# Kernel tuning notes

Hardware: AMD Instinct MI355X
Metric: run time of the kernel (lower is better)

## Reference

```python
import jax, jax.numpy as jnp
import numpy as np

N, E, IN, HID, HEADS, OUT = 20000, 320000, 128, 64, 8, 64
NEG_SLOPE = 0.2  # PyG GATConv default leaky_relu slope


def setup_inputs() -> dict:
    key = jax.random.key(0)
    ks = jax.random.split(key, 12)
    g = lambda k, shape, fan_in: jax.random.normal(k, shape, jnp.float32) / np.sqrt(fan_in)
    return {
        "x": jax.random.normal(ks[0], (N, IN), jnp.float32),
        "edge_index": jax.random.randint(ks[1], (2, E), 0, N, jnp.int32),
        "W1": g(ks[2], (IN, HEADS * HID), IN),
        "att_src1": g(ks[3], (HEADS, HID), HID),
        "att_dst1": g(ks[4], (HEADS, HID), HID),
        "b1": jnp.zeros((HEADS * HID,), jnp.float32),
        "W2": g(ks[5], (HEADS * HID, OUT), HEADS * HID),
        "att_src2": g(ks[6], (1, OUT), OUT),
        "att_dst2": g(ks[7], (1, OUT), OUT),
        "b2": jnp.zeros((OUT,), jnp.float32),
    }


def gat_conv(x, edge_index, W, att_src, att_dst, b, heads, out_ch):
    """PyG-style GATConv with add_self_loops=True, concat=True."""
    n = x.shape[0]
    loop = jnp.arange(n, dtype=edge_index.dtype)
    src = jnp.concatenate([edge_index[0], loop])  # message source nodes
    dst = jnp.concatenate([edge_index[1], loop])  # aggregation targets

    h = (x @ W).reshape(n, heads, out_ch)               # [N,H,C]
    a_s = jnp.sum(h * att_src[None], axis=-1)            # [N,H]
    a_d = jnp.sum(h * att_dst[None], axis=-1)            # [N,H]

    e = jax.nn.leaky_relu(a_s[src] + a_d[dst], NEG_SLOPE)  # [Etot,H]
    # numerically stable edge-softmax over incoming neighborhoods
    m = jax.ops.segment_max(e, dst, num_segments=n)
    m = jnp.where(jnp.isfinite(m), m, 0.0)
    p = jnp.exp(e - m[dst])
    denom = jax.ops.segment_sum(p, dst, num_segments=n)
    alpha = p / denom[dst]                               # [Etot,H]

    out = jax.ops.segment_sum(h[src] * alpha[:, :, None], dst, num_segments=n)  # [N,H,C]
    return out.reshape(n, heads * out_ch) + b


def reference(x, edge_index, W1, att_src1, att_dst1, b1, W2, att_src2, att_dst2, b2):
    h = gat_conv(x, edge_index, W1, att_src1, att_dst1, b1, HEADS, HID)
    h = jax.nn.relu(h)
    out = gat_conv(h, edge_index, W2, att_src2, att_dst2, b2, 1, OUT)
    return out
```

## Files before the change

### kernel.cpp

```cpp
#include <hip/hip_runtime.h>
#include <cstdint>

#define N_NODES 20000
#define N_EDGES 320000
#define ET (N_EDGES + N_NODES)
#define IN_DIM 128
#define HID 64
#define HEADS 8
#define F1 (HEADS * HID)
#define OUT_DIM 64
#define NEG_SLOPE 0.2f
#define NB_SCAN 20

typedef __attribute__((ext_vector_type(8))) short bf16x8;
typedef __attribute__((ext_vector_type(4))) float f32x4;

__device__ __forceinline__ ushort f2bf(float f) {
  uint32_t u = __float_as_uint(f);
  uint32_t r = (u + 0x7fffu + ((u >> 16) & 1u)) >> 16;
  return (ushort)r;
}
__device__ __forceinline__ float bfu_lo(uint32_t p) { return __uint_as_float(p << 16); }
__device__ __forceinline__ float bfu_hi(uint32_t p) { return __uint_as_float(p & 0xffff0000u); }
__device__ __forceinline__ float lrelu(float x) { return x > 0.f ? x : NEG_SLOPE * x; }

__global__ void castT_kernel(const float* __restrict__ in, ushort* __restrict__ out,
                             int R, int C) {
  int idx = blockIdx.x * 256 + threadIdx.x;
  if (idx >= R * C) return;
  int r = idx / C, c = idx - r * C;
  out[(size_t)c * R + r] = f2bf(in[idx]);
}

__global__ void hist_kernel(const int* __restrict__ ei, int* __restrict__ deg) {
  int e = blockIdx.x * 256 + threadIdx.x;
  if (e >= ET) return;
  int dst = (e < N_EDGES) ? ei[N_EDGES + e] : (e - N_EDGES);
  atomicAdd(&deg[dst], 1);
}

__global__ __launch_bounds__(1024) void scan_a(const int* __restrict__ deg,
                                               int* __restrict__ off,
                                               int* __restrict__ bsum) {
  __shared__ int wsum[16];
  int i = blockIdx.x * 1024 + threadIdx.x;
  int lane = threadIdx.x & 63, wid = threadIdx.x >> 6;
  int v = (i < N_NODES) ? deg[i] : 0;
  int s = v;
#pragma unroll
  for (int d = 1; d < 64; d <<= 1) {
    int u = __shfl_up(s, d);
    if (lane >= d) s += u;
  }
  if (lane == 63) wsum[wid] = s;
  __syncthreads();
  if (wid == 0) {
    int ws = (lane < 16) ? wsum[lane] : 0;
#pragma unroll
    for (int d = 1; d < 16; d <<= 1) {
      int u = __shfl_up(ws, d);
      if (lane >= d) ws += u;
    }
    if (lane < 16) wsum[lane] = ws;
  }
  __syncthreads();
  int wbase = (wid > 0) ? wsum[wid - 1] : 0;
  int incl = wbase + s;
  if (i < N_NODES) off[i] = incl - v;
  if (threadIdx.x == 1023) bsum[blockIdx.x] = incl;
}

__global__ void scan_b(const int* __restrict__ bsum, int* __restrict__ boff,
                       int* __restrict__ off) {
  int lane = threadIdx.x;
  int orig = (lane < NB_SCAN) ? bsum[lane] : 0;
  int v = orig;
#pragma unroll
  for (int d = 1; d < 64; d <<= 1) {
    int u = __shfl_up(v, d);
    if (lane >= d) v += u;
  }
  if (lane < NB_SCAN) boff[lane] = v - orig;
  if (lane == NB_SCAN - 1) off[N_NODES] = v;
}

__global__ __launch_bounds__(1024) void scan_c(const int* __restrict__ boff,
                                               int* __restrict__ off,
                                               int* __restrict__ pos) {
  int i = blockIdx.x * 1024 + threadIdx.x;
  if (i >= N_NODES) return;
  int o = off[i] + boff[blockIdx.x];
  off[i] = o;
  pos[i] = o;
}

__global__ void scatter_kernel(const int* __restrict__ ei, int* __restrict__ pos,
                               int* __restrict__ csr_src) {
  int e = blockIdx.x * 256 + threadIdx.x;
  if (e >= ET) return;
  int src, dst;
  if (e < N_EDGES) { src = ei[e]; dst = ei[N_EDGES + e]; }
  else             { src = e - N_EDGES; dst = src; }
  int slot = atomicAdd(&pos[dst], 1);
  csr_src[slot] = src;
}

__device__ __forceinline__ int swz(int r, int kg) { return kg ^ ((r >> 1) & 3); }

template <int WR, int WC, int TM, int TN, int ASD, bool AF32>
__global__ __launch_bounds__(256) void gemm_kernel(
    const void* __restrict__ Av, const ushort* __restrict__ BT,
    ushort* __restrict__ Cb, int M, int K, int NC,
    const float* __restrict__ atts, const float* __restrict__ attd,
    float* __restrict__ asd) {
  constexpr int BM = WR * TM * 16;
  constexpr int BN = WC * TN * 16;
  __shared__ ushort As[BM * 32];
  __shared__ ushort Bs[BN * 32];
  const int t = threadIdx.x;
  const int lane = t & 63, wid = t >> 6;
  const int wr = wid / WC, wc = wid % WC;
  const int m0 = blockIdx.y * BM, n0 = blockIdx.x * BN;
  f32x4 acc[TM][TN] = {};
  const int srow = t >> 2, kg = t & 3;

  for (int k0 = 0; k0 < K; k0 += 32) {
#pragma unroll
    for (int q = 0; q < BM / 64; ++q) {
      int r = srow + 64 * q;
      int gr = m0 + r; if (gr >= M) gr = M - 1;
      bf16x8 v;
      if constexpr (AF32) {
        const float* Ap = (const float*)Av;
        float4 v0 = *reinterpret_cast<const float4*>(&Ap[(size_t)gr * K + k0 + kg * 8]);
        float4 v1 = *reinterpret_cast<const float4*>(&Ap[(size_t)gr * K + k0 + kg * 8 + 4]);
        v[0] = (short)f2bf(v0.x); v[1] = (short)f2bf(v0.y);
        v[2] = (short)f2bf(v0.z); v[3] = (short)f2bf(v0.w);
        v[4] = (short)f2bf(v1.x); v[5] = (short)f2bf(v1.y);
        v[6] = (short)f2bf(v1.z); v[7] = (short)f2bf(v1.w);
      } else {
        v = *reinterpret_cast<const bf16x8*>(&((const ushort*)Av)[(size_t)gr * K + k0 + kg * 8]);
      }
      *reinterpret_cast<bf16x8*>(&As[r * 32 + swz(r, kg) * 8]) = v;
    }
#pragma unroll
    for (int q = 0; q < BN / 64; ++q) {
      int r = srow + 64 * q;
      int gn = n0 + r;
      bf16x8 v = *reinterpret_cast<const bf16x8*>(&BT[(size_t)gn * K + k0 + kg * 8]);
      *reinterpret_cast<bf16x8*>(&Bs[r * 32 + swz(r, kg) * 8]) = v;
    }
    __syncthreads();
    int kq = lane >> 4;
    int rr = lane & 15;
    bf16x8 af[TM], bfv[TN];
#pragma unroll
    for (int i = 0; i < TM; ++i) {
      int r = (wr * TM + i) * 16 + rr;
      af[i] = *reinterpret_cast<const bf16x8*>(&As[r * 32 + swz(r, kq) * 8]);
    }
#pragma unroll
    for (int j = 0; j < TN; ++j) {
      int r = (wc * TN + j) * 16 + rr;
      bfv[j] = *reinterpret_cast<const bf16x8*>(&Bs[r * 32 + swz(r, kq) * 8]);
    }
#pragma unroll
    for (int i = 0; i < TM; ++i)
#pragma unroll
      for (int j = 0; j < TN; ++j)
        acc[i][j] = __builtin_amdgcn_mfma_f32_16x16x32_bf16(af[i], bfv[j], acc[i][j], 0, 0, 0);
    __syncthreads();
  }
  const int cr0 = (lane >> 4) * 4;
  const int cc = lane & 15;
#pragma unroll
  for (int i = 0; i < TM; ++i)
#pragma unroll
    for (int j = 0; j < TN; ++j)
#pragma unroll
      for (int r = 0; r < 4; ++r) {
        int gm = m0 + (wr * TM + i) * 16 + cr0 + r;
        int gn = n0 + (wc * TN + j) * 16 + cc;
        if (gm < M) Cb[(size_t)gm * NC + gn] = f2bf(acc[i][j][r]);
      }
  if constexpr (ASD != 0) {
    static_assert(TN * 16 == 64, "asd fusion needs 64-col wave tile");
    const int hh = (ASD == 1) ? ((n0 + wc * 64) >> 6) : 0;
    float as_v[TN], ad_v[TN];
#pragma unroll
    for (int j = 0; j < TN; ++j) {
      as_v[j] = atts[hh * 64 + j * 16 + cc];
      ad_v[j] = attd[hh * 64 + j * 16 + cc];
    }
#pragma unroll
    for (int i = 0; i < TM; ++i)
#pragma unroll
      for (int r = 0; r < 4; ++r) {
        float ps = 0.f, pd = 0.f;
#pragma unroll
        for (int j = 0; j < TN; ++j) {
          ps += acc[i][j][r] * as_v[j];
          pd += acc[i][j][r] * ad_v[j];
        }
#pragma unroll
        for (int s = 1; s < 16; s <<= 1) {
          ps += __shfl_xor(ps, s);
          pd += __shfl_xor(pd, s);
        }
        int row = m0 + (wr * TM + i) * 16 + cr0 + r;
        if (cc == 0 && row < M) {
          if constexpr (ASD == 1) {
            asd[(size_t)row * 16 + hh] = ps;
            asd[(size_t)row * 16 + 8 + hh] = pd;
          } else {
            asd[(size_t)row * 2 + 0] = ps;
            asd[(size_t)row * 2 + 1] = pd;
          }
        }
      }
  }
}

template <int H, int ASDS, int DOFF>
__global__ void alpha_kernel(const int* __restrict__ off, const int* __restrict__ csrs,
                             const float* __restrict__ asd, float* __restrict__ alpha) {
  int node = blockIdx.x * 4 + (threadIdx.x >> 6);
  if (node >= N_NODES) return;
  int lane = threadIdx.x & 63;
  int h = lane % H;
  int j = lane / H;
  constexpr int STEP = 64 / H;
  int s0 = off[node], s1 = off[node + 1];
  float adst = asd[(size_t)node * ASDS + DOFF + h];
  float mx = -1e30f;
  for (int i = s0 + j; i < s1; i += STEP) {
    float xv = asd[(size_t)csrs[i] * ASDS + h] + adst;
    mx = fmaxf(mx, lrelu(xv));
  }
#pragma unroll
  for (int s = H; s < 64; s <<= 1) mx = fmaxf(mx, __shfl_xor(mx, s));
  float sum = 0.f;
  for (int i = s0 + j; i < s1; i += STEP) {
    float xv = lrelu(asd[(size_t)csrs[i] * ASDS + h] + adst);
    sum += __expf(xv - mx);
  }
#pragma unroll
  for (int s = H; s < 64; s <<= 1) sum += __shfl_xor(sum, s);
  float inv = 1.f / sum;
  for (int i = s0 + j; i < s1; i += STEP) {
    float xv = lrelu(asd[(size_t)csrs[i] * ASDS + h] + adst);
    alpha[(size_t)i * H + h] = __expf(xv - mx) * inv;
  }
}

__global__ __launch_bounds__(64) void agg1_kernel(
    const int* __restrict__ off, const int* __restrict__ csrs,
    const float* __restrict__ alpha, const ushort* __restrict__ H1b,
    const float* __restrict__ b1, ushort* __restrict__ X2b) {
  int bid = blockIdx.x;
  int hg = (bid >= N_NODES) ? 1 : 0;
  int node = bid - hg * N_NODES;
  int lane = threadIdx.x;
  int hl = lane >> 4, fr = lane & 15;
  int head = hg * 4 + hl;
  int s0 = off[node], s1 = off[node + 1];
  const uint2* Hp = reinterpret_cast<const uint2*>(H1b);
  const int uoff = head * 16 + fr;
  float a0 = 0.f, a1 = 0.f, a2 = 0.f, a3 = 0.f;
  int i = s0;
  for (; i + 4 <= s1; i += 4) {
    int sA = csrs[i], sB = csrs[i + 1], sC = csrs[i + 2], sD = csrs[i + 3];
    float lA = alpha[(size_t)i * 8 + head];
    float lB = alpha[(size_t)(i + 1) * 8 + head];
    float lC = alpha[(size_t)(i + 2) * 8 + head];
    float lD = alpha[(size_t)(i + 3) * 8 + head];
    uint2 pA = Hp[(size_t)sA * 128 + uoff];
    uint2 pB = Hp[(size_t)sB * 128 + uoff];
    uint2 pC = Hp[(size_t)sC * 128 + uoff];
    uint2 pD = Hp[(size_t)sD * 128 + uoff];
    a0 += lA * bfu_lo(pA.x) + lB * bfu_lo(pB.x) + lC * bfu_lo(pC.x) + lD * bfu_lo(pD.x);
    a1 += lA * bfu_hi(pA.x) + lB * bfu_hi(pB.x) + lC * bfu_hi(pC.x) + lD * bfu_hi(pD.x);
    a2 += lA * bfu_lo(pA.y) + lB * bfu_lo(pB.y) + lC * bfu_lo(pC.y) + lD * bfu_lo(pD.y);
    a3 += lA * bfu_hi(pA.y) + lB * bfu_hi(pB.y) + lC * bfu_hi(pC.y) + lD * bfu_hi(pD.y);
  }
  for (; i < s1; ++i) {
    int src = csrs[i];
    float l = alpha[(size_t)i * 8 + head];
    uint2 p = Hp[(size_t)src * 128 + uoff];
    a0 += l * bfu_lo(p.x); a1 += l * bfu_hi(p.x);
    a2 += l * bfu_lo(p.y); a3 += l * bfu_hi(p.y);
  }
  int fb = head * 64 + fr * 4;
  float v0 = fmaxf(a0 + b1[fb], 0.f);
  float v1 = fmaxf(a1 + b1[fb + 1], 0.f);
  float v2 = fmaxf(a2 + b1[fb + 2], 0.f);
  float v3 = fmaxf(a3 + b1[fb + 3], 0.f);
  uint2 o;
  o.x = (uint32_t)f2bf(v0) | ((uint32_t)f2bf(v1) << 16);
  o.y = (uint32_t)f2bf(v2) | ((uint32_t)f2bf(v3) << 16);
  reinterpret_cast<uint2*>(X2b)[(size_t)node * 128 + uoff] = o;
}

__global__ __launch_bounds__(256) void agg2_kernel(
    const int* __restrict__ off, const int* __restrict__ csrs,
    const float* __restrict__ alpha, const ushort* __restrict__ H2b,
    const float* __restrict__ b2, float* __restrict__ out) {
  int node = blockIdx.x * 4 + (threadIdx.x >> 6);
  if (node >= N_NODES) return;
  int lane = threadIdx.x & 63;
  int grp = lane >> 4, fr = lane & 15;
  int s0 = off[node], s1 = off[node + 1];
  const uint2* Hp = reinterpret_cast<const uint2*>(H2b);
  float a0 = 0.f, a1 = 0.f, a2 = 0.f, a3 = 0.f;
  for (int i = s0 + grp; i < s1; i += 4) {
    int src = csrs[i];
    float l = alpha[i];
    uint2 p = Hp[(size_t)src * 16 + fr];
    a0 += l * bfu_lo(p.x); a1 += l * bfu_hi(p.x);
    a2 += l * bfu_lo(p.y); a3 += l * bfu_hi(p.y);
  }
#pragma unroll
  for (int d = 16; d < 64; d <<= 1) {
    a0 += __shfl_xor(a0, d);
    a1 += __shfl_xor(a1, d);
    a2 += __shfl_xor(a2, d);
    a3 += __shfl_xor(a3, d);
  }
  if (grp == 0) {
    int fb = fr * 4;
    float4 o;
    o.x = a0 + b2[fb];
    o.y = a1 + b2[fb + 1];
    o.z = a2 + b2[fb + 2];
    o.w = a3 + b2[fb + 3];
    reinterpret_cast<float4*>(out)[(size_t)node * 16 + fr] = o;
  }
}

extern "C" void kernel_launch(void* const* d_in, const int* in_sizes, int n_in,
                              void* d_out, int out_size, void* d_ws, size_t ws_size,
                              hipStream_t stream) {
  const float* x        = (const float*)d_in[0];
  const int*   ei       = (const int*)  d_in[1];
  const float* W1       = (const float*)d_in[2];
  const float* att_src1 = (const float*)d_in[3];
  const float* att_dst1 = (const float*)d_in[4];
  const float* b1       = (const float*)d_in[5];
  const float* W2       = (const float*)d_in[6];
  const float* att_src2 = (const float*)d_in[7];
  const float* att_dst2 = (const float*)d_in[8];
  const float* b2       = (const float*)d_in[9];
  float* out = (float*)d_out;

  char* w = (char*)d_ws;
  auto alloc = [&](size_t bytes) {
    char* p = w;
    w += (bytes + 255) & ~(size_t)255;
    return p;
  };
  ushort* W1T    = (ushort*)alloc((size_t)F1 * IN_DIM * 2);
  ushort* W2T    = (ushort*)alloc((size_t)OUT_DIM * F1 * 2);
  ushort* H1b    = (ushort*)alloc((size_t)N_NODES * F1 * 2);
  ushort* X2b    = (ushort*)alloc((size_t)N_NODES * F1 * 2);
  ushort* H2b    = (ushort*)alloc((size_t)N_NODES * OUT_DIM * 2);
  float* asd1    = (float*)alloc((size_t)N_NODES * 16 * 4);
  float* asd2    = (float*)alloc((size_t)N_NODES * 2 * 4);
  float* alpha1  = (float*)alloc((size_t)ET * 8 * 4);
  float* alpha2  = (float*)alloc((size_t)ET * 4);
  int* deg       = (int*)alloc((size_t)N_NODES * 4);
  int* off       = (int*)alloc((size_t)(N_NODES + 1) * 4);
  int* pos       = (int*)alloc((size_t)N_NODES * 4);
  int* csrsrc    = (int*)alloc((size_t)ET * 4);
  int* bsum      = (int*)alloc((size_t)NB_SCAN * 4);
  int* boff      = (int*)alloc((size_t)NB_SCAN * 4);

  hipMemsetAsync(deg, 0, (size_t)N_NODES * 4, stream);
  hist_kernel<<<(ET + 255) / 256, 256, 0, stream>>>(ei, deg);
  scan_a<<<NB_SCAN, 1024, 0, stream>>>(deg, off, bsum);
  scan_b<<<1, 64, 0, stream>>>(bsum, boff, off);
  scan_c<<<NB_SCAN, 1024, 0, stream>>>(boff, off, pos);
  scatter_kernel<<<(ET + 255) / 256, 256, 0, stream>>>(ei, pos, csrsrc);

  castT_kernel<<<(IN_DIM * F1 + 255) / 256, 256, 0, stream>>>(W1, W1T, IN_DIM, F1);
  castT_kernel<<<(F1 * OUT_DIM + 255) / 256, 256, 0, stream>>>(W2, W2T, F1, OUT_DIM);

  gemm_kernel<2, 2, 4, 4, 1, true>
      <<<dim3(F1 / 128, (N_NODES + 127) / 128), 256, 0, stream>>>(
      x, W1T, H1b, N_NODES, IN_DIM, F1, att_src1, att_dst1, asd1);
  alpha_kernel<8, 16, 8><<<(N_NODES + 3) / 4, 256, 0, stream>>>(off, csrsrc, asd1, alpha1);
  agg1_kernel<<<2 * N_NODES, 64, 0, stream>>>(off, csrsrc, alpha1, H1b, b1, X2b);

  gemm_kernel<4, 1, 1, 4, 2, false>
      <<<dim3(1, (N_NODES + 63) / 64), 256, 0, stream>>>(
      X2b, W2T, H2b, N_NODES, F1, OUT_DIM, att_src2, att_dst2, asd2);
  alpha_kernel<1, 2, 1><<<(N_NODES + 3) / 4, 256, 0, stream>>>(off, csrsrc, asd2, alpha2);
  agg2_kernel<<<(N_NODES + 3) / 4, 256, 0, stream>>>(off, csrsrc, alpha2, H2b, b2, out);
}
```

Baseline: 163.1 us.

## Pre-cast x to bf16, widen agg1 loads to full-row uint4, unroll agg2

Adds a separate kernel that casts x to bf16 once, so the first GEMM loads bf16 directly instead of converting fp32 inside the tile loop. agg1 now uses one 64-lane block per node, each lane loading 16 bytes (8 features), which halves the block count and makes every gather cover a whole contiguous 1 KB row. agg2 is unrolled by two edges per group to get more loads in flight. The cost is an extra kernel launch plus a round trip through a bf16 copy of x, and more registers in agg1.

```diff
diff --git a/kernel.cpp b/kernel.cpp
--- a/kernel.cpp
+++ b/kernel.cpp
@@ -24,6 +24,15 @@
 __device__ __forceinline__ float bfu_hi(uint32_t p) { return __uint_as_float(p & 0xffff0000u); }
 __device__ __forceinline__ float lrelu(float x) { return x > 0.f ? x : NEG_SLOPE * x; }
 
+__global__ void cast_kernel(const float* __restrict__ in, ushort* __restrict__ out, int n4) {
+  int i = blockIdx.x * 256 + threadIdx.x;
+  if (i >= n4) return;
+  float4 v = reinterpret_cast<const float4*>(in)[i];
+  ushort4 o;
+  o.x = f2bf(v.x); o.y = f2bf(v.y); o.z = f2bf(v.z); o.w = f2bf(v.w);
+  reinterpret_cast<ushort4*>(out)[i] = o;
+}
+
 __global__ void castT_kernel(const float* __restrict__ in, ushort* __restrict__ out,
                              int R, int C) {
   int idx = blockIdx.x * 256 + threadIdx.x;
@@ -107,9 +116,9 @@
 
 __device__ __forceinline__ int swz(int r, int kg) { return kg ^ ((r >> 1) & 3); }
 
-template <int WR, int WC, int TM, int TN, int ASD, bool AF32>
+template <int WR, int WC, int TM, int TN, int ASD>
 __global__ __launch_bounds__(256) void gemm_kernel(
-    const void* __restrict__ Av, const ushort* __restrict__ BT,
+    const ushort* __restrict__ A, const ushort* __restrict__ BT,
     ushort* __restrict__ Cb, int M, int K, int NC,
     const float* __restrict__ atts, const float* __restrict__ attd,
     float* __restrict__ asd) {
@@ -129,18 +138,7 @@
     for (int q = 0; q < BM / 64; ++q) {
       int r = srow + 64 * q;
       int gr = m0 + r; if (gr >= M) gr = M - 1;
-      bf16x8 v;
-      if constexpr (AF32) {
-        const float* Ap = (const float*)Av;
-        float4 v0 = *reinterpret_cast<const float4*>(&Ap[(size_t)gr * K + k0 + kg * 8]);
-        float4 v1 = *reinterpret_cast<const float4*>(&Ap[(size_t)gr * K + k0 + kg * 8 + 4]);
-        v[0] = (short)f2bf(v0.x); v[1] = (short)f2bf(v0.y);
-        v[2] = (short)f2bf(v0.z); v[3] = (short)f2bf(v0.w);
-        v[4] = (short)f2bf(v1.x); v[5] = (short)f2bf(v1.y);
-        v[6] = (short)f2bf(v1.z); v[7] = (short)f2bf(v1.w);
-      } else {
-        v = *reinterpret_cast<const bf16x8*>(&((const ushort*)Av)[(size_t)gr * K + k0 + kg * 8]);
-      }
+      bf16x8 v = *reinterpret_cast<const bf16x8*>(&A[(size_t)gr * K + k0 + kg * 8]);
       *reinterpret_cast<bf16x8*>(&As[r * 32 + swz(r, kg) * 8]) = v;
     }
 #pragma unroll
@@ -257,16 +255,13 @@
     const int* __restrict__ off, const int* __restrict__ csrs,
     const float* __restrict__ alpha, const ushort* __restrict__ H1b,
     const float* __restrict__ b1, ushort* __restrict__ X2b) {
-  int bid = blockIdx.x;
-  int hg = (bid >= N_NODES) ? 1 : 0;
-  int node = bid - hg * N_NODES;
+  int node = blockIdx.x;
   int lane = threadIdx.x;
-  int hl = lane >> 4, fr = lane & 15;
-  int head = hg * 4 + hl;
+  int head = lane >> 3;
   int s0 = off[node], s1 = off[node + 1];
-  const uint2* Hp = reinterpret_cast<const uint2*>(H1b);
-  const int uoff = head * 16 + fr;
+  const uint4* Hp = reinterpret_cast<const uint4*>(H1b);
   float a0 = 0.f, a1 = 0.f, a2 = 0.f, a3 = 0.f;
+  float a4 = 0.f, a5 = 0.f, a6 = 0.f, a7 = 0.f;
   int i = s0;
   for (; i + 4 <= s1; i += 4) {
     int sA = csrs[i], sB = csrs[i + 1], sC = csrs[i + 2], sD = csrs[i + 3];
@@ -274,31 +269,40 @@
     float lB = alpha[(size_t)(i + 1) * 8 + head];
     float lC = alpha[(size_t)(i + 2) * 8 + head];
     float lD = alpha[(size_t)(i + 3) * 8 + head];
-    uint2 pA = Hp[(size_t)sA * 128 + uoff];
-    uint2 pB = Hp[(size_t)sB * 128 + uoff];
-    uint2 pC = Hp[(size_t)sC * 128 + uoff];
-    uint2 pD = Hp[(size_t)sD * 128 + uoff];
+    uint4 pA = Hp[(size_t)sA * 64 + lane];
+    uint4 pB = Hp[(size_t)sB * 64 + lane];
+    uint4 pC = Hp[(size_t)sC * 64 + lane];
+    uint4 pD = Hp[(size_t)sD * 64 + lane];
     a0 += lA * bfu_lo(pA.x) + lB * bfu_lo(pB.x) + lC * bfu_lo(pC.x) + lD * bfu_lo(pD.x);
     a1 += lA * bfu_hi(pA.x) + lB * bfu_hi(pB.x) + lC * bfu_hi(pC.x) + lD * bfu_hi(pD.x);
     a2 += lA * bfu_lo(pA.y) + lB * bfu_lo(pB.y) + lC * bfu_lo(pC.y) + lD * bfu_lo(pD.y);
     a3 += lA * bfu_hi(pA.y) + lB * bfu_hi(pB.y) + lC * bfu_hi(pC.y) + lD * bfu_hi(pD.y);
+    a4 += lA * bfu_lo(pA.z) + lB * bfu_lo(pB.z) + lC * bfu_lo(pC.z) + lD * bfu_lo(pD.z);
+    a5 += lA * bfu_hi(pA.z) + lB * bfu_hi(pB.z) + lC * bfu_hi(pC.z) + lD * bfu_hi(pD.z);
+    a6 += lA * bfu_lo(pA.w) + lB * bfu_lo(pB.w) + lC * bfu_lo(pC.w) + lD * bfu_lo(pD.w);
+    a7 += lA * bfu_hi(pA.w) + lB * bfu_hi(pB.w) + lC * bfu_hi(pC.w) + lD * bfu_hi(pD.w);
   }
   for (; i < s1; ++i) {
     int src = csrs[i];
     float l = alpha[(size_t)i * 8 + head];
-    uint2 p = Hp[(size_t)src * 128 + uoff];
+    uint4 p = Hp[(size_t)src * 64 + lane];
     a0 += l * bfu_lo(p.x); a1 += l * bfu_hi(p.x);
     a2 += l * bfu_lo(p.y); a3 += l * bfu_hi(p.y);
-  }
-  int fb = head * 64 + fr * 4;
-  float v0 = fmaxf(a0 + b1[fb], 0.f);
-  float v1 = fmaxf(a1 + b1[fb + 1], 0.f);
-  float v2 = fmaxf(a2 + b1[fb + 2], 0.f);
-  float v3 = fmaxf(a3 + b1[fb + 3], 0.f);
-  uint2 o;
+    a4 += l * bfu_lo(p.z); a5 += l * bfu_hi(p.z);
+    a6 += l * bfu_lo(p.w); a7 += l * bfu_hi(p.w);
+  }
+  float4 bA = reinterpret_cast<const float4*>(b1)[lane * 2];
+  float4 bB = reinterpret_cast<const float4*>(b1)[lane * 2 + 1];
+  float v0 = fmaxf(a0 + bA.x, 0.f), v1 = fmaxf(a1 + bA.y, 0.f);
+  float v2 = fmaxf(a2 + bA.z, 0.f), v3 = fmaxf(a3 + bA.w, 0.f);
+  float v4 = fmaxf(a4 + bB.x, 0.f), v5 = fmaxf(a5 + bB.y, 0.f);
+  float v6 = fmaxf(a6 + bB.z, 0.f), v7 = fmaxf(a7 + bB.w, 0.f);
+  uint4 o;
   o.x = (uint32_t)f2bf(v0) | ((uint32_t)f2bf(v1) << 16);
   o.y = (uint32_t)f2bf(v2) | ((uint32_t)f2bf(v3) << 16);
-  reinterpret_cast<uint2*>(X2b)[(size_t)node * 128 + uoff] = o;
+  o.z = (uint32_t)f2bf(v4) | ((uint32_t)f2bf(v5) << 16);
+  o.w = (uint32_t)f2bf(v6) | ((uint32_t)f2bf(v7) << 16);
+  reinterpret_cast<uint4*>(X2b)[(size_t)node * 64 + lane] = o;
 }
 
 __global__ __launch_bounds__(256) void agg2_kernel(
@@ -312,7 +316,18 @@
   int s0 = off[node], s1 = off[node + 1];
   const uint2* Hp = reinterpret_cast<const uint2*>(H2b);
   float a0 = 0.f, a1 = 0.f, a2 = 0.f, a3 = 0.f;
-  for (int i = s0 + grp; i < s1; i += 4) {
+  int i = s0 + grp;
+  for (; i + 4 < s1; i += 8) {
+    int srcA = csrs[i], srcB = csrs[i + 4];
+    float lA = alpha[i], lB = alpha[i + 4];
+    uint2 pA = Hp[(size_t)srcA * 16 + fr];
+    uint2 pB = Hp[(size_t)srcB * 16 + fr];
+    a0 += lA * bfu_lo(pA.x) + lB * bfu_lo(pB.x);
+    a1 += lA * bfu_hi(pA.x) + lB * bfu_hi(pB.x);
+    a2 += lA * bfu_lo(pA.y) + lB * bfu_lo(pB.y);
+    a3 += lA * bfu_hi(pA.y) + lB * bfu_hi(pB.y);
+  }
+  if (i < s1) {
     int src = csrs[i];
     float l = alpha[i];
     uint2 p = Hp[(size_t)src * 16 + fr];
@@ -358,6 +373,7 @@
     w += (bytes + 255) & ~(size_t)255;
     return p;
   };
+  ushort* xb     = (ushort*)alloc((size_t)N_NODES * IN_DIM * 2);
   ushort* W1T    = (ushort*)alloc((size_t)F1 * IN_DIM * 2);
   ushort* W2T    = (ushort*)alloc((size_t)OUT_DIM * F1 * 2);
   ushort* H1b    = (ushort*)alloc((size_t)N_NODES * F1 * 2);
@@ -381,16 +397,17 @@
   scan_c<<<NB_SCAN, 1024, 0, stream>>>(boff, off, pos);
   scatter_kernel<<<(ET + 255) / 256, 256, 0, stream>>>(ei, pos, csrsrc);
 
+  cast_kernel<<<(N_NODES * IN_DIM / 4 + 255) / 256, 256, 0, stream>>>(x, xb, N_NODES * IN_DIM / 4);
   castT_kernel<<<(IN_DIM * F1 + 255) / 256, 256, 0, stream>>>(W1, W1T, IN_DIM, F1);
   castT_kernel<<<(F1 * OUT_DIM + 255) / 256, 256, 0, stream>>>(W2, W2T, F1, OUT_DIM);
 
-  gemm_kernel<2, 2, 4, 4, 1, true>
+  gemm_kernel<2, 2, 4, 4, 1>
       <<<dim3(F1 / 128, (N_NODES + 127) / 128), 256, 0, stream>>>(
-      x, W1T, H1b, N_NODES, IN_DIM, F1, att_src1, att_dst1, asd1);
+      xb, W1T, H1b, N_NODES, IN_DIM, F1, att_src1, att_dst1, asd1);
   alpha_kernel<8, 16, 8><<<(N_NODES + 3) / 4, 256, 0, stream>>>(off, csrsrc, asd1, alpha1);
-  agg1_kernel<<<2 * N_NODES, 64, 0, stream>>>(off, csrsrc, alpha1, H1b, b1, X2b);
-
-  gemm_kernel<4, 1, 1, 4, 2, false>
+  agg1_kernel<<<N_NODES, 64, 0, stream>>>(off, csrsrc, alpha1, H1b, b1, X2b);
+
+  gemm_kernel<4, 1, 1, 4, 2>
       <<<dim3(1, (N_NODES + 63) / 64), 256, 0, stream>>>(
       X2b, W2T, H2b, N_NODES, F1, OUT_DIM, att_src2, att_dst2, asd2);
   alpha_kernel<1, 2, 1><<<(N_NODES + 3) / 4, 256, 0, stream>>>(off, csrsrc, asd2, alpha2);
```

Result: slower. 168.1 us (+3.1%).
